# Kernel tuning notes

Measured on AMD Instinct MI355X. Metric: run time of the kernel, lower is better.

Reference implementation:

```python
import jax, jax.numpy as jnp
import numpy as np

B, L, D = 2, 4096, 1024
H, HD = 16, D // 16
W = 256          # window_size
C = 256          # chunk/block size (== W, so each block sees prev + current block)
NC = L // C
SCALE = HD ** -0.5


def complex_linear(z, Wr, Wi):
    # z: [..., D, 2]; W*: [out, in] (torch Linear convention y = x @ W^T)
    xr, xi = z[..., 0], z[..., 1]
    yr = jnp.einsum('...i,oi->...o', xr, Wr) - jnp.einsum('...i,oi->...o', xi, Wi)
    yi = jnp.einsum('...i,oi->...o', xr, Wi) + jnp.einsum('...i,oi->...o', xi, Wr)
    return jnp.stack([yr, yi], axis=-1)


def _heads(x):
    # [B, L, D, 2] -> [B, H, NC, C, HD, 2]
    return x.reshape(B, L, H, HD, 2).transpose(0, 2, 1, 3, 4).reshape(B, H, NC, C, HD, 2)


def _band_mask():
    # block c, query local qi (global i = c*C + qi), key local kj over [prev block | cur block]
    # global j = (c-1)*C + kj ; valid iff 0 <= j <= i and i - j < W
    c = jnp.arange(NC)[:, None, None]
    qi = jnp.arange(C)[None, :, None]
    kj = jnp.arange(2 * C)[None, None, :]
    i = c * C + qi
    j = (c - 1) * C + kj
    return (j >= 0) & (j <= i) & (i - j < W)  # [NC, C, 2C]


def setup_inputs() -> dict:
    key = jax.random.key(0)
    ks = jax.random.split(key, 9)
    s = D ** -0.5
    inp = {'z': jax.random.normal(ks[0], (B, L, D, 2), jnp.float32)}
    names = ['Wq_r', 'Wq_i', 'Wk_r', 'Wk_i', 'Wv_r', 'Wv_i', 'Wo_r', 'Wo_i']
    for n, k in zip(names, ks[1:]):
        inp[n] = jax.random.normal(k, (D, D), jnp.float32) * s
    return inp


def reference(z, Wq_r, Wq_i, Wk_r, Wk_i, Wv_r, Wv_i, Wo_r, Wo_i):
    q = _heads(complex_linear(z, Wq_r, Wq_i))  # [B,H,NC,C,HD,2]
    k = _heads(complex_linear(z, Wk_r, Wk_i))
    v = _heads(complex_linear(z, Wv_r, Wv_i))

    def with_prev(x):  # [B,H,NC,C,HD,2] -> [B,H,NC,2C,HD,2] (prev block | cur block)
        prev = jnp.concatenate([jnp.zeros_like(x[:, :, :1]), x[:, :, :-1]], axis=2)
        return jnp.concatenate([prev, x], axis=3)

    kc = with_prev(k)
    vc = with_prev(v)

    # Re(q * conj(k)) = qr*kr + qi*ki
    scores = (jnp.einsum('bhncd,bhnkd->bhnck', q[..., 0], kc[..., 0])
              + jnp.einsum('bhncd,bhnkd->bhnck', q[..., 1], kc[..., 1])) * SCALE
    scores = jnp.where(_band_mask()[None, None], scores, -jnp.inf)
    w = jax.nn.softmax(scores, axis=-1)  # [B,H,NC,C,2C]

    out_r = jnp.einsum('bhnck,bhnkd->bhncd', w, vc[..., 0])
    out_i = jnp.einsum('bhnck,bhnkd->bhncd', w, vc[..., 1])
    out = jnp.stack([out_r, out_i], axis=-1)           # [B,H,NC,C,HD,2]
    out = out.reshape(B, H, L, HD, 2).transpose(0, 2, 1, 3, 4).reshape(B, L, D, 2)
    return complex_linear(out, Wo_r, Wo_i)
```

## Files before the change

kernel.cpp:

```cpp
#include <hip/hip_runtime.h>
#include <hip/hip_bf16.h>
#include <stdint.h>


typedef __attribute__((ext_vector_type(8))) short bf16x8;
typedef __attribute__((ext_vector_type(8))) unsigned short u16x8;
typedef __attribute__((ext_vector_type(4))) float f32x4;

#define PA_SCALE 0.125f
#define UNR _Pragma("unroll")

__device__ __forceinline__ unsigned short f2bf(float f) {
  unsigned int u = __builtin_bit_cast(unsigned int, f);
  u += 0x7fffu + ((u >> 16) & 1u);
  return (unsigned short)(u >> 16);
}

#define GLD16(gp, lp)                                          \
  __builtin_amdgcn_global_load_lds(                            \
      (const __attribute__((address_space(1))) void*)(gp),     \
      (__attribute__((address_space(3))) void*)(lp), 16, 0, 0)

__global__ __launch_bounds__(256) void pa_pack_A(const float* __restrict__ z,
                                                 unsigned short* __restrict__ A1) {
  int idx = (blockIdx.x * 256 + threadIdx.x) * 8;
  int m = idx >> 10, d = idx & 1023;
  const float2* zp = (const float2*)z + idx;
  u16x8 re, im;
  UNR for (int j = 0; j < 8; ++j) {
    float2 f = zp[j];
    re[j] = f2bf(f.x);
    im[j] = f2bf(f.y);
  }
  *(u16x8*)(A1 + (size_t)m * 2048 + d)        = re;
  *(u16x8*)(A1 + (size_t)m * 2048 + 1024 + d) = im;
}

__global__ __launch_bounds__(256) void pa_pack_B(
    const float* __restrict__ Wq_r, const float* __restrict__ Wq_i,
    const float* __restrict__ Wk_r, const float* __restrict__ Wk_i,
    const float* __restrict__ Wv_r, const float* __restrict__ Wv_i,
    const float* __restrict__ Wo_r, const float* __restrict__ Wo_i,
    unsigned short* __restrict__ Bp) {
  int idx = (blockIdx.x * 256 + threadIdx.x) * 8;
  int n = idx >> 10, d = idx & 1023;
  int proj = n >> 11, part = (n >> 10) & 1, o = n & 1023;
  const float* Wr; const float* Wi;
  if (proj == 0)      { Wr = Wq_r; Wi = Wq_i; }
  else if (proj == 1) { Wr = Wk_r; Wi = Wk_i; }
  else if (proj == 2) { Wr = Wv_r; Wi = Wv_i; }
  else                { Wr = Wo_r; Wi = Wo_i; }
  const float* pr = Wr + (size_t)o * 1024 + d;
  const float* pi = Wi + (size_t)o * 1024 + d;
  u16x8 lo, hi;
  UNR for (int j = 0; j < 8; ++j) {
    float r = pr[j], im = pi[j];
    if (part == 0) { lo[j] = f2bf(r);  hi[j] = f2bf(-im); }
    else           { lo[j] = f2bf(im); hi[j] = f2bf(r);  }
  }
  *(u16x8*)(Bp + (size_t)n * 2048 + d)        = lo;
  *(u16x8*)(Bp + (size_t)n * 2048 + 1024 + d) = hi;
}

#define BARR()                              \
  do {                                      \
    __builtin_amdgcn_s_barrier();           \
    __builtin_amdgcn_sched_barrier(0);      \
  } while (0)

#define READ_A(P, MH)                                                         \
  UNR for (int i = 0; i < 4; ++i)                                             \
    UNR for (int ks = 0; ks < 2; ++ks)                                        \
      af[i][ks] = *(const bf16x8*)&lds[P][MH][aoff + i * 1024 +               \
                                              ((ks * 32 + koff) ^ cxor)];

#define READ_B(P, NH, DST)                                                    \
  UNR for (int j = 0; j < 2; ++j)                                             \
    UNR for (int ks = 0; ks < 2; ++ks)                                        \
      DST[j][ks] = *(const bf16x8*)&lds[P][2 + (NH)][boff + j * 1024 +        \
                                                     ((ks * 32 + koff) ^ cxor)];

#define MFMA_Q(MB, NB, BF)                                                    \
  UNR for (int ks = 0; ks < 2; ++ks)                                          \
    UNR for (int i = 0; i < 4; ++i)                                           \
      UNR for (int j = 0; j < 2; ++j)                                         \
        acc[(MB) + i][(NB) + j] = __builtin_amdgcn_mfma_f32_16x16x32_bf16(    \
            af[i][ks], BF[j][ks], acc[(MB) + i][(NB) + j], 0, 0, 0);

#define TILE(P, T)                                                            \
  {                                                                           \
    READ_A(P, 0);                                                             \
    READ_B(P, 0, b0);                                                         \
    stageB(0, (T) + 1);                                                       \
    BARR();                                                                   \
    __builtin_amdgcn_s_setprio(1);                                            \
    MFMA_Q(0, 0, b0);                                                         \
    __builtin_amdgcn_s_setprio(0);                                            \
    BARR();                                                                   \
    READ_B(P, 1, b1);                                                         \
    stageA(0, (T) + 2);                                                       \
    BARR();                                                                   \
    __builtin_amdgcn_s_setprio(1);                                            \
    MFMA_Q(0, 2, b1);                                                         \
    __builtin_amdgcn_s_setprio(0);                                            \
    BARR();                                                                   \
    READ_A(P, 1);                                                             \
    stageB(1, (T) + 2);                                                       \
    BARR();                                                                   \
    __builtin_amdgcn_s_setprio(1);                                            \
    MFMA_Q(4, 2, b1);                                                         \
    __builtin_amdgcn_s_setprio(0);                                            \
    BARR();                                                                   \
    stageA(1, (T) + 2);                                                       \
    BARR();                                                                   \
    __builtin_amdgcn_s_setprio(1);                                            \
    MFMA_Q(4, 0, b0);                                                         \
    __builtin_amdgcn_s_setprio(0);                                            \
    asm volatile("s_waitcnt vmcnt(6)" ::: "memory");                          \
    __builtin_amdgcn_sched_barrier(0);                                        \
    BARR();                                                                   \
  }

template <int EPI>
__global__ __launch_bounds__(512, 2) void pa_gemm8(
    const unsigned short* __restrict__ A,
    const unsigned short* __restrict__ B,
    void* __restrict__ Cout, int K, int N) {
  __shared__ unsigned short lds[2][4][128 * 64];

  const int tid = threadIdx.x;
  const int lane = tid & 63, wid = tid >> 6;
  const int wm = wid >> 2, wn = wid & 3;
  const int lr = lane & 15, lh = lane >> 4;

  const int nwg = gridDim.x * gridDim.y;
  const int wg = blockIdx.y * gridDim.x + blockIdx.x;
  const int cpx = nwg >> 3;
  const int swz = (wg & 7) * cpx + (wg >> 3);
  const int bx = swz % gridDim.x, by = swz / gridDim.x;
  const int tm0 = by * 256, tn0 = bx * 256;

  const int NT = K >> 6;

  const int srow = lane >> 3;
  const int scolS = ((lane & 7) ^ srow) * 8;

  auto stageA = [&](int half, int ts) {
    int t = ts < NT ? ts : ts - NT;
    const unsigned short* g0 = A + (size_t)(tm0 + half * 128) * K + t * 64 + scolS;
    unsigned short* l0 = &lds[ts & 1][half][0];
    UNR for (int c = 0; c < 2; ++c) {
      int chunk = wid * 2 + c;
      GLD16(g0 + (size_t)(chunk * 8 + srow) * K, l0 + chunk * 512);
    }
  };
  auto stageB = [&](int half, int ts) {
    int t = ts < NT ? ts : ts - NT;
    const unsigned short* g0 = B + (size_t)(tn0 + half * 128) * K + t * 64 + scolS;
    unsigned short* l0 = &lds[ts & 1][2 + half][0];
    UNR for (int c = 0; c < 2; ++c) {
      int chunk = wid * 2 + c;
      GLD16(g0 + (size_t)(chunk * 8 + srow) * K, l0 + chunk * 512);
    }
  };

  const int aoff = (wm * 64 + lr) * 64;
  const int boff = (wn * 32 + lr) * 64;
  const int koff = lh * 8;
  const int cxor = (lr & 7) * 8;

  f32x4 acc[8][4];
  f32x4 zero4 = {0.f, 0.f, 0.f, 0.f};
  UNR for (int i = 0; i < 8; ++i)
    UNR for (int j = 0; j < 4; ++j) acc[i][j] = zero4;

  bf16x8 af[4][2], b0[2][2], b1[2][2];

  stageA(0, 0); stageB(0, 0); stageB(1, 0); stageA(1, 0);
  stageA(0, 1); stageB(1, 1); stageA(1, 1);
  asm volatile("s_waitcnt vmcnt(6)" ::: "memory");
  __builtin_amdgcn_sched_barrier(0);
  __builtin_amdgcn_s_barrier();
  __builtin_amdgcn_sched_barrier(0);

  for (int t = 0; t < NT; t += 2) {
    TILE(0, t);
    TILE(1, t + 1);
  }

  UNR for (int mh = 0; mh < 2; ++mh)
    UNR for (int i = 0; i < 4; ++i)
      UNR for (int nh = 0; nh < 2; ++nh)
        UNR for (int j = 0; j < 2; ++j)
          UNR for (int r = 0; r < 4; ++r) {
            int row = tm0 + mh * 128 + wm * 64 + i * 16 + lh * 4 + r;
            int col = tn0 + nh * 128 + wn * 32 + j * 16 + lr;
            float v = acc[mh * 4 + i][nh * 2 + j][r];
            if (EPI == 0) {
              ((unsigned short*)Cout)[(size_t)row * N + col] = f2bf(v);
            } else {
              int part = col >> 10, dd = col & 1023;
              ((float*)Cout)[((size_t)row * 1024 + dd) * 2 + part] = v;
            }
          }
}

#define QK1(SI)                                                               \
  UNR for (int kk = 0; kk < 2; ++kk)                                          \
    UNR for (int f = 0; f < 4; ++f) {                                         \
      bf16x8 br = *(const bf16x8*)&Ks[0][f * 16 + lr][kk * 32 + lh * 8];      \
      bf16x8 bi = *(const bf16x8*)&Ks[1][f * 16 + lr][kk * 32 + lh * 8];      \
      sac[SI][f] = __builtin_amdgcn_mfma_f32_16x16x32_bf16(qfr[kk], br,       \
                                                           sac[SI][f], 0, 0, 0); \
      sac[SI][f] = __builtin_amdgcn_mfma_f32_16x16x32_bf16(qfi[kk], bi,       \
                                                           sac[SI][f], 0, 0, 0); \
    }

#define PW1(SI)                                                               \
  UNR for (int f = 0; f < 4; ++f)                                             \
    UNR for (int r = 0; r < 4; ++r)                                           \
      Ps[wv][lh * 4 + r][f * 16 + lr] = f2bf(sac[SI][f][r]);

#define PV1()                                                                 \
  {                                                                           \
    bf16x8 pa0 = *(const bf16x8*)&Ps[wv][lr][lh * 8];                         \
    bf16x8 pa1 = *(const bf16x8*)&Ps[wv][lr][32 + lh * 8];                    \
    UNR for (int kk = 0; kk < 2; ++kk) {                                      \
      bf16x8 pak = kk ? pa1 : pa0;                                            \
      UNR for (int fc = 0; fc < 4; ++fc) {                                    \
        bf16x8 vr = *(const bf16x8*)&Vts[0][fc * 16 + lr][kk * 32 + lh * 8];  \
        bf16x8 vi = *(const bf16x8*)&Vts[1][fc * 16 + lr][kk * 32 + lh * 8];  \
        oac[0][fc] = __builtin_amdgcn_mfma_f32_16x16x32_bf16(pak, vr,         \
                                                             oac[0][fc], 0, 0, 0); \
        oac[1][fc] = __builtin_amdgcn_mfma_f32_16x16x32_bf16(pak, vi,         \
                                                             oac[1][fc], 0, 0, 0); \
      }                                                                       \
    }                                                                         \
  }

__global__ __launch_bounds__(512) void pa_attn(const unsigned short* __restrict__ C1,
                                               unsigned short* __restrict__ A2) {
  __shared__ unsigned short Ks[2][64][72];
  __shared__ unsigned short Vts[2][64][72];
  __shared__ unsigned short Ps[8][16][72];

  int bid = blockIdx.x;
  int half = bid & 1, nc = (bid >> 1) & 15, h = (bid >> 5) & 15, b = bid >> 9;
  int tid = threadIdx.x;
  int l = tid & 63, wv = tid >> 6;
  int lr = l & 15, lh = l >> 4;
  int base = wv >> 2;

  const int C1LD = 6144;
  const int rowB = b * 4096;
  const int colQr = h * 64,        colQi = 1024 + h * 64;
  const int colKr = 2048 + h * 64, colKi = 3072 + h * 64;
  const int colVr = 4096 + h * 64, colVi = 5120 + h * 64;
  const int q0 = half * 128;
  const int qw = q0 + wv * 16;

  bf16x8 qfr[2], qfi[2];
  {
    const unsigned short* pr = C1 + (size_t)(rowB + nc * 256 + qw + lr) * C1LD + colQr;
    const unsigned short* pi = C1 + (size_t)(rowB + nc * 256 + qw + lr) * C1LD + colQi;
    qfr[0] = *(const bf16x8*)(pr + lh * 8);
    qfr[1] = *(const bf16x8*)(pr + 32 + lh * 8);
    qfi[0] = *(const bf16x8*)(pi + lh * 8);
    qfi[1] = *(const bf16x8*)(pi + 32 + lh * 8);
  }

  f32x4 zero4 = {0.f, 0.f, 0.f, 0.f};
  f32x4 sac[5][4];
#pragma unroll
  for (int c = 0; c < 5; ++c)
#pragma unroll
    for (int f = 0; f < 4; ++f) sac[c][f] = zero4;

#pragma unroll
  for (int c = 0; c < 6; ++c) {
    __syncthreads();
#pragma unroll
    for (int s = 0; s < 2; ++s) {
      int seg = s * 512 + tid;
      int arr = seg >> 9, row = (seg >> 3) & 63, sg = seg & 7;
      int kj = q0 + c * 64 + row;
      int tok = (nc - 1) * 256 + kj; if (tok < 0) tok = 0;
      const unsigned short* src =
          C1 + (size_t)(rowB + tok) * C1LD + (arr ? colKi : colKr) + sg * 8;
      *(bf16x8*)&Ks[arr][row][sg * 8] = *(const bf16x8*)src;
    }
    __syncthreads();
    if (wv < 4) { if (c < 5) { QK1(c); } }
    else        { if (c >= 1) { QK1(c - 1); } }
  }

  float mx[4] = {-1e30f, -1e30f, -1e30f, -1e30f};
#pragma unroll
  for (int si = 0; si < 5; ++si)
#pragma unroll
    for (int f = 0; f < 4; ++f)
#pragma unroll
      for (int r = 0; r < 4; ++r) {
        int qi_ = qw + lh * 4 + r;
        int kj  = q0 + (si + base) * 64 + f * 16 + lr;
        bool valid = (kj > qi_) && (kj <= qi_ + 256) && (nc > 0 || kj >= 256);
        float s = valid ? sac[si][f][r] * PA_SCALE : -1e30f;
        sac[si][f][r] = s;
        mx[r] = fmaxf(mx[r], s);
      }
#pragma unroll
  for (int r = 0; r < 4; ++r)
#pragma unroll
    for (int d = 1; d < 16; d <<= 1) mx[r] = fmaxf(mx[r], __shfl_xor(mx[r], d));

  float sm[4] = {0.f, 0.f, 0.f, 0.f};
#pragma unroll
  for (int si = 0; si < 5; ++si)
#pragma unroll
    for (int f = 0; f < 4; ++f)
#pragma unroll
      for (int r = 0; r < 4; ++r) {
        float p = __expf(sac[si][f][r] - mx[r]);
        sac[si][f][r] = p;
        sm[r] += p;
      }
#pragma unroll
  for (int r = 0; r < 4; ++r)
#pragma unroll
    for (int d = 1; d < 16; d <<= 1) sm[r] += __shfl_xor(sm[r], d);
  float inv[4];
#pragma unroll
  for (int r = 0; r < 4; ++r) inv[r] = 1.0f / sm[r];

  f32x4 oac[2][4];
#pragma unroll
  for (int p = 0; p < 2; ++p)
#pragma unroll
    for (int f = 0; f < 4; ++f) oac[p][f] = zero4;

#pragma unroll
  for (int c = 0; c < 6; ++c) {
    __syncthreads();
#pragma unroll
    for (int s = 0; s < 2; ++s) {
      int seg = s * 512 + tid;
      int arr = seg >> 9, row = (seg >> 3) & 63, sg = seg & 7;
      int kj = q0 + c * 64 + row;
      int tok = (nc - 1) * 256 + kj; if (tok < 0) tok = 0;
      const unsigned short* src =
          C1 + (size_t)(rowB + tok) * C1LD + (arr ? colVi : colVr) + sg * 8;
      bf16x8 v = *(const bf16x8*)src;
#pragma unroll
      for (int j = 0; j < 8; ++j) Vts[arr][sg * 8 + j][row] = (unsigned short)v[j];
    }
    if (wv < 4) { if (c < 5) { PW1(c); } }
    else        { if (c >= 1) { PW1(c - 1); } }
    __syncthreads();
    if (wv < 4) { if (c < 5) { PV1(); } }
    else        { if (c >= 1) { PV1(); } }
  }

#pragma unroll
  for (int fc = 0; fc < 4; ++fc)
#pragma unroll
    for (int r = 0; r < 4; ++r) {
      int m  = rowB + nc * 256 + qw + lh * 4 + r;
      int hd = fc * 16 + lr;
      A2[(size_t)m * 2048 + h * 64 + hd]        = f2bf(oac[0][fc][r] * inv[r]);
      A2[(size_t)m * 2048 + 1024 + h * 64 + hd] = f2bf(oac[1][fc][r] * inv[r]);
    }
}

extern "C" void kernel_launch(void* const* d_in, const int* in_sizes, int n_in,
                              void* d_out, int out_size, void* d_ws, size_t ws_size,
                              hipStream_t stream) {
  const float* z = (const float*)d_in[0];
  unsigned short* A1 = (unsigned short*)d_ws;
  unsigned short* Bp = (unsigned short*)((char*)d_ws + 33554432ull);
  unsigned short* C1 = (unsigned short*)((char*)d_ws + 67108864ull);
  float* out = (float*)d_out;

  pa_pack_A<<<4096, 256, 0, stream>>>(z, A1);
  pa_pack_B<<<4096, 256, 0, stream>>>(
      (const float*)d_in[1], (const float*)d_in[2],
      (const float*)d_in[3], (const float*)d_in[4],
      (const float*)d_in[5], (const float*)d_in[6],
      (const float*)d_in[7], (const float*)d_in[8], Bp);
  pa_gemm8<0><<<dim3(24, 32), 512, 0, stream>>>(A1, Bp, C1, 2048, 6144);
  pa_attn<<<1024, 512, 0, stream>>>(C1, A1);
  pa_gemm8<1><<<dim3(8, 32), 512, 0, stream>>>(A1, Bp + (size_t)6144 * 2048, out,
                                               2048, 2048);
}
```

Measured before the change: 384.2 us.

## Load V alongside K into full LDS buffer and drop PV-phase barriers

V tiles for all six key chunks are now loaded and transposed into a six-slot shared buffer during the QK loop, using the same token row address as K. The PV phase then runs per wave with no block barriers and no further global loads. This removes a second pass of global loads and twelve syncthreads. The cost is a much larger LDS footprint, which likely limits occupancy to one block per CU.

```diff
diff --git a/kernel.cpp b/kernel.cpp
--- a/kernel.cpp
+++ b/kernel.cpp
@@ -216,32 +216,10 @@
                                                            sac[SI][f], 0, 0, 0); \
     }
 
-#define PW1(SI)                                                               \
-  UNR for (int f = 0; f < 4; ++f)                                             \
-    UNR for (int r = 0; r < 4; ++r)                                           \
-      Ps[wv][lh * 4 + r][f * 16 + lr] = f2bf(sac[SI][f][r]);
-
-#define PV1()                                                                 \
-  {                                                                           \
-    bf16x8 pa0 = *(const bf16x8*)&Ps[wv][lr][lh * 8];                         \
-    bf16x8 pa1 = *(const bf16x8*)&Ps[wv][lr][32 + lh * 8];                    \
-    UNR for (int kk = 0; kk < 2; ++kk) {                                      \
-      bf16x8 pak = kk ? pa1 : pa0;                                            \
-      UNR for (int fc = 0; fc < 4; ++fc) {                                    \
-        bf16x8 vr = *(const bf16x8*)&Vts[0][fc * 16 + lr][kk * 32 + lh * 8];  \
-        bf16x8 vi = *(const bf16x8*)&Vts[1][fc * 16 + lr][kk * 32 + lh * 8];  \
-        oac[0][fc] = __builtin_amdgcn_mfma_f32_16x16x32_bf16(pak, vr,         \
-                                                             oac[0][fc], 0, 0, 0); \
-        oac[1][fc] = __builtin_amdgcn_mfma_f32_16x16x32_bf16(pak, vi,         \
-                                                             oac[1][fc], 0, 0, 0); \
-      }                                                                       \
-    }                                                                         \
-  }
-
 __global__ __launch_bounds__(512) void pa_attn(const unsigned short* __restrict__ C1,
                                                unsigned short* __restrict__ A2) {
   __shared__ unsigned short Ks[2][64][72];
-  __shared__ unsigned short Vts[2][64][72];
+  __shared__ unsigned short Vts[6][2][64][72];
   __shared__ unsigned short Ps[8][16][72];
 
   int bid = blockIdx.x;
@@ -285,9 +263,12 @@
       int arr = seg >> 9, row = (seg >> 3) & 63, sg = seg & 7;
       int kj = q0 + c * 64 + row;
       int tok = (nc - 1) * 256 + kj; if (tok < 0) tok = 0;
-      const unsigned short* src =
-          C1 + (size_t)(rowB + tok) * C1LD + (arr ? colKi : colKr) + sg * 8;
-      *(bf16x8*)&Ks[arr][row][sg * 8] = *(const bf16x8*)src;
+      const unsigned short* rp = C1 + (size_t)(rowB + tok) * C1LD;
+      *(bf16x8*)&Ks[arr][row][sg * 8] =
+          *(const bf16x8*)(rp + (arr ? colKi : colKr) + sg * 8);
+      bf16x8 v = *(const bf16x8*)(rp + (arr ? colVi : colVr) + sg * 8);
+#pragma unroll
+      for (int j = 0; j < 8; ++j) Vts[c][arr][sg * 8 + j][row] = (unsigned short)v[j];
     }
     __syncthreads();
     if (wv < 4) { if (c < 5) { QK1(c); } }
@@ -338,26 +319,31 @@
 #pragma unroll
     for (int f = 0; f < 4; ++f) oac[p][f] = zero4;
 
-#pragma unroll
-  for (int c = 0; c < 6; ++c) {
-    __syncthreads();
-#pragma unroll
-    for (int s = 0; s < 2; ++s) {
-      int seg = s * 512 + tid;
-      int arr = seg >> 9, row = (seg >> 3) & 63, sg = seg & 7;
-      int kj = q0 + c * 64 + row;
-      int tok = (nc - 1) * 256 + kj; if (tok < 0) tok = 0;
-      const unsigned short* src =
-          C1 + (size_t)(rowB + tok) * C1LD + (arr ? colVi : colVr) + sg * 8;
-      bf16x8 v = *(const bf16x8*)src;
-#pragma unroll
-      for (int j = 0; j < 8; ++j) Vts[arr][sg * 8 + j][row] = (unsigned short)v[j];
-    }
-    if (wv < 4) { if (c < 5) { PW1(c); } }
-    else        { if (c >= 1) { PW1(c - 1); } }
-    __syncthreads();
-    if (wv < 4) { if (c < 5) { PV1(); } }
-    else        { if (c >= 1) { PV1(); } }
+  const unsigned short* vb = &Vts[0][0][0][0] + base * 9216;
+
+#pragma unroll
+  for (int si = 0; si < 5; ++si) {
+#pragma unroll
+    for (int f = 0; f < 4; ++f)
+#pragma unroll
+      for (int r = 0; r < 4; ++r)
+        Ps[wv][lh * 4 + r][f * 16 + lr] = f2bf(sac[si][f][r]);
+
+    bf16x8 pa0 = *(const bf16x8*)&Ps[wv][lr][lh * 8];
+    bf16x8 pa1 = *(const bf16x8*)&Ps[wv][lr][32 + lh * 8];
+#pragma unroll
+    for (int kk = 0; kk < 2; ++kk) {
+      bf16x8 pak = kk ? pa1 : pa0;
+#pragma unroll
+      for (int fc = 0; fc < 4; ++fc) {
+        const unsigned short* pvr =
+            vb + si * 9216 + (fc * 16 + lr) * 72 + kk * 32 + lh * 8;
+        bf16x8 vr = *(const bf16x8*)pvr;
+        bf16x8 vi = *(const bf16x8*)(pvr + 4608);
+        oac[0][fc] = __builtin_amdgcn_mfma_f32_16x16x32_bf16(pak, vr, oac[0][fc], 0, 0, 0);
+        oac[1][fc] = __builtin_amdgcn_mfma_f32_16x16x32_bf16(pak, vi, oac[1][fc], 0, 0, 0);
+      }
+    }
   }
 
 #pragma unroll
```

Measured after the change: 389.0 us. No clear change (+1.3%).
